# Performance work log

Hardware: AMD Instinct MI355X
Metric: run time of the kernel (lower is better)

The kernel has to match this reference:

```python
import jax, jax.numpy as jnp
import numpy as np
import math

EPSILON = 1e-15
N, D = 1048576, 128

def setup_inputs() -> dict:
    key = jax.random.key(0)
    k_x, k_mu, k_a, k_eps = jax.random.split(key, 4)
    X = jax.random.normal(k_x, (N, D), dtype=jnp.float32)
    # mu = (rand(D) - 0.5) * 2.0  as in __init__
    mu = (jax.random.uniform(k_mu, (D,), dtype=jnp.float32) - 0.5) * 2.0
    # sigma starts as identity; make a well-conditioned SPD matrix (as after EM updates)
    A = jax.random.normal(k_a, (D, D), dtype=jnp.float32) * 0.05
    sigma = jnp.eye(D, dtype=jnp.float32) + A @ A.T
    # epsilon property: (rand(D,D) - 0.5) * 1e-15, sampled once here (deterministic)
    eps = (jax.random.uniform(k_eps, (D, D), dtype=jnp.float32) - 0.5) * EPSILON
    return {"X": X, "mu": mu, "sigma": sigma, "eps": eps}

def reference(X, mu, sigma, eps):
    D_ = X.shape[1]
    log_two_pi_dims = D_ * (jnp.log(jnp.float32(2.0)) + jnp.log(jnp.float32(math.pi)))
    sig = sigma + eps
    inv_sigma = jnp.linalg.pinv(sig)
    _, log_det_sigma = jnp.linalg.slogdet(sig)
    log_den = 0.5 * (log_two_pi_dims + log_det_sigma)
    diff = X - mu  # [N, D]
    # batched quadratic form: diff @ inv_sigma . diff, summed over D
    quad = jnp.einsum('nd,de,ne->n', diff, inv_sigma, diff)  # [N]
    log_prob = -0.5 * quad - log_den  # [N]
    # nll=True path: return -log_prob, shape [N, 1] to match torch.cat of (1,1) blocks
    return (-log_prob)[:, None]
```

## Files before the change

kernel.cpp:

```cpp
#include <hip/hip_runtime.h>
#include <hip/hip_bf16.h>

typedef __bf16 bf16x8 __attribute__((ext_vector_type(8)));
typedef float f32x4 __attribute__((ext_vector_type(4)));

#define DIM 128
#define LOG_2PI 1.8378770664093453f
#define X0C 0.36f

__device__ __forceinline__ unsigned short f2bf(float f) {
    unsigned int u = __float_as_uint(f);
    u += 0x7FFFu + ((u >> 16) & 1u);
    return (unsigned short)(u >> 16);
}
__device__ __forceinline__ float bfu(unsigned short u) {
    return __uint_as_float((unsigned int)u << 16);
}
__device__ __forceinline__ int foidx(int r, int c) {
    return ((r >> 3) << 10) + (c << 3) + (r & 7);
}

__device__ __forceinline__ void mm_acc8(const unsigned short* __restrict__ Ps,
                                        const unsigned short* __restrict__ Qs,
                                        f32x4 acc[2][4], int wr, int tcb, int l15, int l4)
{
#pragma unroll
    for (int kk = 0; kk < 4; ++kk) {
        const int kc = kk * 4 + l4;
        const bf16x8 a0 = *reinterpret_cast<const bf16x8*>(Ps + (kc << 10) + ((wr * 32 + l15) << 3));
        const bf16x8 a1 = *reinterpret_cast<const bf16x8*>(Ps + (kc << 10) + ((wr * 32 + 16 + l15) << 3));
#pragma unroll
        for (int c = 0; c < 4; ++c) {
            const bf16x8 b = *reinterpret_cast<const bf16x8*>(Qs + (kc << 10) + (((tcb + c) * 16 + l15) << 3));
            acc[0][c] = __builtin_amdgcn_mfma_f32_16x16x32_bf16(a0, b, acc[0][c], 0, 0, 0);
            acc[1][c] = __builtin_amdgcn_mfma_f32_16x16x32_bf16(a1, b, acc[1][c], 0, 0, 0);
        }
    }
}

__device__ __forceinline__ void zacc(f32x4 acc[2][4]) {
#pragma unroll
    for (int rt = 0; rt < 2; ++rt)
#pragma unroll
        for (int c = 0; c < 4; ++c) { acc[rt][c][0] = 0.f; acc[rt][c][1] = 0.f; acc[rt][c][2] = 0.f; acc[rt][c][3] = 0.f; }
}

__device__ __forceinline__ void wb8s(unsigned short* __restrict__ C, f32x4 acc[2][4],
                                     int wr, int tcb, int l15, int l4, float sgn)
{
#pragma unroll
    for (int rt = 0; rt < 2; ++rt) {
        const int r0 = wr * 32 + rt * 16 + l4 * 4;
#pragma unroll
        for (int c = 0; c < 4; ++c) {
            ushort4 p;
            p.x = f2bf(sgn * acc[rt][c][0]); p.y = f2bf(sgn * acc[rt][c][1]);
            p.z = f2bf(sgn * acc[rt][c][2]); p.w = f2bf(sgn * acc[rt][c][3]);
            *reinterpret_cast<ushort4*>(&C[foidx(r0, (tcb + c) * 16 + l15)]) = p;
        }
    }
}

__global__ __launch_bounds__(512) void gm_setup(
    const float* __restrict__ sigma, const float* __restrict__ eps,
    unsigned short* __restrict__ wsB, float* __restrict__ wsScal)
{
    __shared__ __align__(16) unsigned short B0[16384];
    __shared__ __align__(16) unsigned short B1[16384];
    __shared__ __align__(16) unsigned short B2[16384];
    __shared__ __align__(16) unsigned short B3[16384];
    __shared__ float sv[8];

    const int tid  = threadIdx.x;
    const int lane = tid & 63;
    const int w    = tid >> 6;
    const int l15  = lane & 15;
    const int l4   = lane >> 4;
    const int wr   = w >> 1;
    const int tcb  = (w & 1) * 4;

#pragma unroll
    for (int h = 0; h < 4; ++h) {
        const int v = tid + h * 512;
        const int c = v & 127, rb = v >> 7;
        ushort4 s0, s1, x0q, x1q;
#pragma unroll
        for (int j = 0; j < 8; ++j) {
            const int r = rb * 8 + j;
            const float s = sigma[r * DIM + c] + eps[r * DIM + c];
            const float x = ((r == c) ? (2.0f * X0C) : 0.0f) - (X0C * X0C) * s;
            if (j < 4) { ((unsigned short*)&s0)[j] = f2bf(s); ((unsigned short*)&x0q)[j] = f2bf(x); }
            else       { ((unsigned short*)&s1)[j-4] = f2bf(s); ((unsigned short*)&x1q)[j-4] = f2bf(x); }
        }
        const int f = v * 8;
        *reinterpret_cast<ushort4*>(&B0[f])     = s0;
        *reinterpret_cast<ushort4*>(&B0[f + 4]) = s1;
        *reinterpret_cast<ushort4*>(&B2[f])     = x0q;
        *reinterpret_cast<ushort4*>(&B2[f + 4]) = x1q;
    }
    __syncthreads();

    for (int it = 0; it < 5; ++it) {
        unsigned short* Xc = (it & 1) ? B1 : B2;
        unsigned short* Xo = (it & 1) ? B2 : B1;
        f32x4 acc[2][4];
        zacc(acc);
        mm_acc8(B0, Xc, acc, wr, tcb, l15, l4);
        wb8s(B3, acc, wr, tcb, l15, l4, -1.0f);
        __syncthreads();
        f32x4 a2[2][4];
#pragma unroll
        for (int rt = 0; rt < 2; ++rt) {
            const int r0 = wr * 32 + rt * 16 + l4 * 4;
#pragma unroll
            for (int c = 0; c < 4; ++c) {
                const ushort4 x4 = *reinterpret_cast<const ushort4*>(&Xc[foidx(r0, (tcb + c) * 16 + l15)]);
                a2[rt][c][0] = 2.0f * bfu(x4.x); a2[rt][c][1] = 2.0f * bfu(x4.y);
                a2[rt][c][2] = 2.0f * bfu(x4.z); a2[rt][c][3] = 2.0f * bfu(x4.w);
            }
        }
        mm_acc8(Xc, B3, a2, wr, tcb, l15, l4);
        wb8s(Xo, a2, wr, tcb, l15, l4, 1.0f);
        __syncthreads();
    }

    float tsum = 0.0f;
#pragma unroll
    for (int h = 0; h < 4; ++h) {
        const int v = tid + h * 512;
        const int c = v & 127, rb = v >> 7;
        const int f = v * 8;
#pragma unroll
        for (int q = 0; q < 2; ++q) {
            const ushort4 wq = *reinterpret_cast<const ushort4*>(&B1[f + q * 4]);
            ushort4 mv;
#pragma unroll
            for (int j = 0; j < 4; ++j) {
                const int r = rb * 8 + q * 4 + j;
                const float wv = bfu(((const unsigned short*)&wq)[j]);
                const float mf = ((r == c) ? 1.0f : 0.0f) - wv;
                ((unsigned short*)&mv)[j] = f2bf(mf);
                tsum += 0.5f * mf * mf + ((r == c) ? mf : 0.0f);
            }
            *reinterpret_cast<ushort4*>(&B2[f + q * 4]) = mv;
            *reinterpret_cast<ushort4*>(&B3[f + q * 4]) = mv;
            *reinterpret_cast<ushort4*>(&wsB[f + q * 4]) = wq;
        }
    }
    __syncthreads();

    ushort4 pold[2][4];
    {
        f32x4 acc[2][4];
        zacc(acc);
        mm_acc8(B2, B3, acc, wr, tcb, l15, l4);
#pragma unroll
        for (int rt = 0; rt < 2; ++rt) {
            const int r0 = wr * 32 + rt * 16 + l4 * 4;
#pragma unroll
            for (int c = 0; c < 4; ++c) {
                const int f = foidx(r0, (tcb + c) * 16 + l15);
                const ushort4 m4 = *reinterpret_cast<const ushort4*>(&B2[f]);
                ushort4 nw;
#pragma unroll
                for (int j4 = 0; j4 < 4; ++j4) {
                    const float x = acc[rt][c][j4];
                    ((unsigned short*)&nw)[j4] = f2bf(x);
                    tsum += x * bfu(((const unsigned short*)&m4)[j4]) * 0.333333333f + x * x * 0.25f;
                }
                *reinterpret_cast<ushort4*>(&B0[f]) = nw;
                pold[rt][c] = nw;
            }
        }
        __syncthreads();
    }

    {
        f32x4 acc[2][4];
        zacc(acc);
        mm_acc8(B2, B0, acc, wr, tcb, l15, l4);
#pragma unroll
        for (int rt = 0; rt < 2; ++rt) {
            const int r0 = wr * 32 + rt * 16 + l4 * 4;
#pragma unroll
            for (int c = 0; c < 4; ++c) {
                const int f = foidx(r0, (tcb + c) * 16 + l15);
                ushort4 nw;
#pragma unroll
                for (int j4 = 0; j4 < 4; ++j4) {
                    const float x = acc[rt][c][j4];
                    ((unsigned short*)&nw)[j4] = f2bf(x);
                    tsum += x * bfu(((const unsigned short*)&pold[rt][c])[j4]) * 0.2f + x * x * 0.166666667f;
                }
                *reinterpret_cast<ushort4*>(&B3[f]) = nw;
                pold[rt][c] = nw;
            }
        }
        __syncthreads();
    }

    {
        f32x4 acc[2][4];
        zacc(acc);
        mm_acc8(B2, B3, acc, wr, tcb, l15, l4);
#pragma unroll
        for (int rt = 0; rt < 2; ++rt)
#pragma unroll
            for (int c = 0; c < 4; ++c)
#pragma unroll
                for (int j4 = 0; j4 < 4; ++j4) {
                    const float x = acc[rt][c][j4];
                    tsum += x * bfu(((const unsigned short*)&pold[rt][c])[j4]) * 0.142857143f + x * x * 0.125f;
                }
    }

    {
        float s = tsum;
#pragma unroll
        for (int off = 1; off < 64; off <<= 1) s += __shfl_xor(s, off, 64);
        if (lane == 0) sv[w] = s;
    }
    __syncthreads();
    if (tid == 0) {
        float tot = 0.f;
        for (int i = 0; i < 8; ++i) tot += sv[i];
        wsScal[0] = 0.5f * ((float)DIM * LOG_2PI + tot);
    }
}

__global__ __launch_bounds__(256) void gm_main(
    const float* __restrict__ X, const float* __restrict__ mu,
    const __hip_bfloat16* __restrict__ wsB, const float* __restrict__ wsScal,
    float* __restrict__ out, int ntiles)
{
    __shared__ __hip_bfloat16 sB[16 * 1024];
    __shared__ unsigned short sA[64 * 128];
    __shared__ float s_mu[DIM];

    const int tid  = threadIdx.x;
    const int lane = tid & 63;
    const int wave = tid >> 6;
    const int l15  = lane & 15;
    const int l4   = lane >> 4;

    {
        const float4* bg = reinterpret_cast<const float4*>(wsB);
        float4* bs = reinterpret_cast<float4*>(sB);
#pragma unroll
        for (int i = 0; i < 8; ++i) bs[tid + i * 256] = bg[tid + i * 256];
        if (tid < DIM) s_mu[tid] = mu[tid];
    }
    const float logden = wsScal[0];
    __syncthreads();

    for (int t = blockIdx.x; t < ntiles; t += gridDim.x) {
        const float4* xg = reinterpret_cast<const float4*>(X + (size_t)t * (64 * DIM));
#pragma unroll
        for (int i = 0; i < 8; ++i) {
            const int idx = tid + i * 256;
            const int r  = idx >> 5;
            const int c4 = idx & 31;
            float4 v = xg[idx];
            v.x -= s_mu[c4 * 4 + 0];
            v.y -= s_mu[c4 * 4 + 1];
            v.z -= s_mu[c4 * 4 + 2];
            v.w -= s_mu[c4 * 4 + 3];
            ushort4 b;
            b.x = f2bf(v.x); b.y = f2bf(v.y); b.z = f2bf(v.z); b.w = f2bf(v.w);
            char* p = (char*)sA + r * 256 + ((((c4 >> 1) ^ (r & 7)) << 4) | ((c4 & 1) << 3));
            *reinterpret_cast<ushort4*>(p) = b;
        }
        __syncthreads();

        f32x4 acc[8];
#pragma unroll
        for (int c = 0; c < 8; ++c) { acc[c][0] = 0.f; acc[c][1] = 0.f; acc[c][2] = 0.f; acc[c][3] = 0.f; }

        const int arow = wave * 16 + l15;
        const char* aBase = (const char*)sA + arow * 256;
#pragma unroll
        for (int kk = 0; kk < 4; ++kk) {
            const int kchunk = kk * 4 + l4;
            bf16x8 af = *reinterpret_cast<const bf16x8*>(aBase + ((kchunk ^ (arow & 7)) << 4));
            const __hip_bfloat16* bbase = sB + kchunk * 1024 + l15 * 8;
#pragma unroll
            for (int c = 0; c < 8; ++c) {
                bf16x8 bf = *reinterpret_cast<const bf16x8*>(bbase + c * 128);
                acc[c] = __builtin_amdgcn_mfma_f32_16x16x32_bf16(af, bf, acc[c], 0, 0, 0);
            }
        }

        float q0 = 0.f, q1 = 0.f, q2 = 0.f, q3 = 0.f;
#pragma unroll
        for (int c = 0; c < 8; ++c) {
            const int d = c * 16 + l15;
#pragma unroll
            for (int j = 0; j < 4; ++j) {
                const int r = wave * 16 + l4 * 4 + j;
                const int byt = r * 256 +
                    ((((d >> 3) ^ (r & 7)) << 4) | (((d >> 2) & 1) << 3) | ((d & 3) << 1));
                const unsigned short u = *reinterpret_cast<const unsigned short*>((const char*)sA + byt);
                const float df = __uint_as_float((unsigned int)u << 16);
                if (j == 0) q0 += acc[c][0] * df;
                else if (j == 1) q1 += acc[c][1] * df;
                else if (j == 2) q2 += acc[c][2] * df;
                else q3 += acc[c][3] * df;
            }
        }
#pragma unroll
        for (int off = 1; off < 16; off <<= 1) {
            q0 += __shfl_xor(q0, off, 64);
            q1 += __shfl_xor(q1, off, 64);
            q2 += __shfl_xor(q2, off, 64);
            q3 += __shfl_xor(q3, off, 64);
        }
        if (l15 == 0) {
            float4 o;
            o.x = 0.5f * q0 + logden;
            o.y = 0.5f * q1 + logden;
            o.z = 0.5f * q2 + logden;
            o.w = 0.5f * q3 + logden;
            *reinterpret_cast<float4*>(out + (size_t)t * 64 + wave * 16 + l4 * 4) = o;
        }
        __syncthreads();
    }
}

extern "C" void kernel_launch(void* const* d_in, const int* in_sizes, int n_in,
                              void* d_out, int out_size, void* d_ws, size_t ws_size,
                              hipStream_t stream) {
    const float* X     = (const float*)d_in[0];
    const float* mu    = (const float*)d_in[1];
    const float* sigma = (const float*)d_in[2];
    const float* eps   = (const float*)d_in[3];
    float* out = (float*)d_out;

    unsigned short* wsB = (unsigned short*)d_ws;
    float* wsScal = (float*)((char*)d_ws + 32768);

    const int N = in_sizes[0] / DIM;
    const int ntiles = N / 64;

    hipLaunchKernelGGL(gm_setup, dim3(1), dim3(512), 0, stream, sigma, eps, wsB, wsScal);

    const int grid = ntiles < 768 ? ntiles : 768;
    hipLaunchKernelGGL(gm_main, dim3(grid), dim3(256), 0, stream,
                       X, mu, (const __hip_bfloat16*)wsB, wsScal, out, ntiles);
}
```

Baseline: 124.6 us.

## Use inverse square root factor so quadratic form becomes sum of squares

The setup kernel now runs a coupled Newton-Schulz iteration that produces a scaled inverse square root of sigma instead of the inverse, and stores that as the GEMM operand. The main kernel then computes the quadratic form as the squared norm of the MFMA output, dropping the second pass that re-read diff from shared memory. Each wave now loads and uses its own 16-row slice of shared memory, which removes the block-wide barriers per tile. The risk is precision: the coupled iteration is done in bf16 with only four steps, and the log-determinant series is now fed a different matrix.

```diff
diff --git a/kernel.cpp b/kernel.cpp
--- a/kernel.cpp
+++ b/kernel.cpp
@@ -6,7 +6,8 @@
 
 #define DIM 128
 #define LOG_2PI 1.8378770664093453f
-#define X0C 0.36f
+#define INVLAM 0.3846153846f
+#define RSLAM  0.6201736729f
 
 __device__ __forceinline__ unsigned short f2bf(float f) {
     unsigned int u = __float_as_uint(f);
@@ -45,8 +46,8 @@
         for (int c = 0; c < 4; ++c) { acc[rt][c][0] = 0.f; acc[rt][c][1] = 0.f; acc[rt][c][2] = 0.f; acc[rt][c][3] = 0.f; }
 }
 
-__device__ __forceinline__ void wb8s(unsigned short* __restrict__ C, f32x4 acc[2][4],
-                                     int wr, int tcb, int l15, int l4, float sgn)
+__device__ __forceinline__ void wb8(unsigned short* __restrict__ C, f32x4 acc[2][4],
+                                    int wr, int tcb, int l15, int l4)
 {
 #pragma unroll
     for (int rt = 0; rt < 2; ++rt) {
@@ -54,8 +55,8 @@
 #pragma unroll
         for (int c = 0; c < 4; ++c) {
             ushort4 p;
-            p.x = f2bf(sgn * acc[rt][c][0]); p.y = f2bf(sgn * acc[rt][c][1]);
-            p.z = f2bf(sgn * acc[rt][c][2]); p.w = f2bf(sgn * acc[rt][c][3]);
+            p.x = f2bf(acc[rt][c][0]); p.y = f2bf(acc[rt][c][1]);
+            p.z = f2bf(acc[rt][c][2]); p.w = f2bf(acc[rt][c][3]);
             *reinterpret_cast<ushort4*>(&C[foidx(r0, (tcb + c) * 16 + l15)]) = p;
         }
     }
@@ -83,92 +84,118 @@
     for (int h = 0; h < 4; ++h) {
         const int v = tid + h * 512;
         const int c = v & 127, rb = v >> 7;
-        ushort4 s0, s1, x0q, x1q;
+        ushort4 a0q, a1q, z0q, z1q;
 #pragma unroll
         for (int j = 0; j < 8; ++j) {
             const int r = rb * 8 + j;
-            const float s = sigma[r * DIM + c] + eps[r * DIM + c];
-            const float x = ((r == c) ? (2.0f * X0C) : 0.0f) - (X0C * X0C) * s;
-            if (j < 4) { ((unsigned short*)&s0)[j] = f2bf(s); ((unsigned short*)&x0q)[j] = f2bf(x); }
-            else       { ((unsigned short*)&s1)[j-4] = f2bf(s); ((unsigned short*)&x1q)[j-4] = f2bf(x); }
+            const float a = (sigma[r * DIM + c] + eps[r * DIM + c]) * INVLAM;
+            const float z = 0.5f * (((r == c) ? 3.0f : 0.0f) - a);
+            if (j < 4) { ((unsigned short*)&a0q)[j] = f2bf(a); ((unsigned short*)&z0q)[j] = f2bf(z); }
+            else       { ((unsigned short*)&a1q)[j-4] = f2bf(a); ((unsigned short*)&z1q)[j-4] = f2bf(z); }
         }
         const int f = v * 8;
-        *reinterpret_cast<ushort4*>(&B0[f])     = s0;
-        *reinterpret_cast<ushort4*>(&B0[f + 4]) = s1;
-        *reinterpret_cast<ushort4*>(&B2[f])     = x0q;
-        *reinterpret_cast<ushort4*>(&B2[f + 4]) = x1q;
+        *reinterpret_cast<ushort4*>(&B0[f])     = a0q;
+        *reinterpret_cast<ushort4*>(&B0[f + 4]) = a1q;
+        *reinterpret_cast<ushort4*>(&B1[f])     = z0q;
+        *reinterpret_cast<ushort4*>(&B1[f + 4]) = z1q;
     }
     __syncthreads();
 
-    for (int it = 0; it < 5; ++it) {
-        unsigned short* Xc = (it & 1) ? B1 : B2;
-        unsigned short* Xo = (it & 1) ? B2 : B1;
-        f32x4 acc[2][4];
-        zacc(acc);
-        mm_acc8(B0, Xc, acc, wr, tcb, l15, l4);
-        wb8s(B3, acc, wr, tcb, l15, l4, -1.0f);
-        __syncthreads();
-        f32x4 a2[2][4];
+    for (int it = 0; it < 4; ++it) {
+        unsigned short* Zc = (it & 1) ? B2 : B1;
+        unsigned short* Zo = (it & 1) ? B1 : B2;
+        f32x4 acc[2][4];
+        zacc(acc);
+        mm_acc8(Zc, Zc, acc, wr, tcb, l15, l4);
+        wb8(Zo, acc, wr, tcb, l15, l4);
+        __syncthreads();
+        f32x4 av[2][4];
+        zacc(av);
+        mm_acc8(B0, Zo, av, wr, tcb, l15, l4);
+        {
+            f32x4 tp[2][4];
+#pragma unroll
+            for (int rt = 0; rt < 2; ++rt) {
+                const int r0 = wr * 32 + rt * 16 + l4 * 4;
+#pragma unroll
+                for (int c = 0; c < 4; ++c) {
+                    const int col = (tcb + c) * 16 + l15;
+#pragma unroll
+                    for (int j = 0; j < 4; ++j)
+                        tp[rt][c][j] = 0.5f * (((r0 + j == col) ? 3.0f : 0.0f) - av[rt][c][j]);
+                }
+            }
+            wb8(B3, tp, wr, tcb, l15, l4);
+        }
+        __syncthreads();
+        f32x4 az[2][4];
+        zacc(az);
+        mm_acc8(Zc, B3, az, wr, tcb, l15, l4);
+        wb8(Zo, az, wr, tcb, l15, l4);
+        __syncthreads();
+    }
+
+    for (int i = tid; i < 2048; i += 512) {
+        const ushort4 za = *reinterpret_cast<const ushort4*>(&B1[i * 8]);
+        const ushort4 zb = *reinterpret_cast<const ushort4*>(&B1[i * 8 + 4]);
+        ushort4 ba, bb;
+        ba.x = f2bf(bfu(za.x) * RSLAM); ba.y = f2bf(bfu(za.y) * RSLAM);
+        ba.z = f2bf(bfu(za.z) * RSLAM); ba.w = f2bf(bfu(za.w) * RSLAM);
+        bb.x = f2bf(bfu(zb.x) * RSLAM); bb.y = f2bf(bfu(zb.y) * RSLAM);
+        bb.z = f2bf(bfu(zb.z) * RSLAM); bb.w = f2bf(bfu(zb.w) * RSLAM);
+        *reinterpret_cast<ushort4*>(&B2[i * 8])     = ba;
+        *reinterpret_cast<ushort4*>(&B2[i * 8 + 4]) = bb;
+        *reinterpret_cast<ushort4*>(&wsB[i * 8])     = ba;
+        *reinterpret_cast<ushort4*>(&wsB[i * 8 + 4]) = bb;
+    }
+    __syncthreads();
+
+    float tsum = 0.0f;
+    ushort4 pold[2][4];
+    {
+        f32x4 acc[2][4];
+        zacc(acc);
+        mm_acc8(B2, B2, acc, wr, tcb, l15, l4);
 #pragma unroll
         for (int rt = 0; rt < 2; ++rt) {
             const int r0 = wr * 32 + rt * 16 + l4 * 4;
 #pragma unroll
             for (int c = 0; c < 4; ++c) {
-                const ushort4 x4 = *reinterpret_cast<const ushort4*>(&Xc[foidx(r0, (tcb + c) * 16 + l15)]);
-                a2[rt][c][0] = 2.0f * bfu(x4.x); a2[rt][c][1] = 2.0f * bfu(x4.y);
-                a2[rt][c][2] = 2.0f * bfu(x4.z); a2[rt][c][3] = 2.0f * bfu(x4.w);
-            }
-        }
-        mm_acc8(Xc, B3, a2, wr, tcb, l15, l4);
-        wb8s(Xo, a2, wr, tcb, l15, l4, 1.0f);
-        __syncthreads();
-    }
-
-    float tsum = 0.0f;
-#pragma unroll
-    for (int h = 0; h < 4; ++h) {
-        const int v = tid + h * 512;
-        const int c = v & 127, rb = v >> 7;
-        const int f = v * 8;
-#pragma unroll
-        for (int q = 0; q < 2; ++q) {
-            const ushort4 wq = *reinterpret_cast<const ushort4*>(&B1[f + q * 4]);
-            ushort4 mv;
-#pragma unroll
-            for (int j = 0; j < 4; ++j) {
-                const int r = rb * 8 + q * 4 + j;
-                const float wv = bfu(((const unsigned short*)&wq)[j]);
-                const float mf = ((r == c) ? 1.0f : 0.0f) - wv;
-                ((unsigned short*)&mv)[j] = f2bf(mf);
-                tsum += 0.5f * mf * mf + ((r == c) ? mf : 0.0f);
-            }
-            *reinterpret_cast<ushort4*>(&B2[f + q * 4]) = mv;
-            *reinterpret_cast<ushort4*>(&B3[f + q * 4]) = mv;
-            *reinterpret_cast<ushort4*>(&wsB[f + q * 4]) = wq;
-        }
-    }
-    __syncthreads();
-
-    ushort4 pold[2][4];
-    {
-        f32x4 acc[2][4];
-        zacc(acc);
-        mm_acc8(B2, B3, acc, wr, tcb, l15, l4);
+                const int col = (tcb + c) * 16 + l15;
+                const int f = foidx(r0, col);
+                ushort4 mv;
+#pragma unroll
+                for (int j = 0; j < 4; ++j) {
+                    const float mf = ((r0 + j == col) ? 1.0f : 0.0f) - acc[rt][c][j];
+                    ((unsigned short*)&mv)[j] = f2bf(mf);
+                    tsum += 0.5f * mf * mf + ((r0 + j == col) ? mf : 0.0f);
+                }
+                *reinterpret_cast<ushort4*>(&B0[f]) = mv;
+                *reinterpret_cast<ushort4*>(&B3[f]) = mv;
+                pold[rt][c] = mv;
+            }
+        }
+        __syncthreads();
+    }
+
+    {
+        f32x4 acc[2][4];
+        zacc(acc);
+        mm_acc8(B0, B3, acc, wr, tcb, l15, l4);
 #pragma unroll
         for (int rt = 0; rt < 2; ++rt) {
             const int r0 = wr * 32 + rt * 16 + l4 * 4;
 #pragma unroll
             for (int c = 0; c < 4; ++c) {
                 const int f = foidx(r0, (tcb + c) * 16 + l15);
-                const ushort4 m4 = *reinterpret_cast<const ushort4*>(&B2[f]);
                 ushort4 nw;
 #pragma unroll
                 for (int j4 = 0; j4 < 4; ++j4) {
                     const float x = acc[rt][c][j4];
                     ((unsigned short*)&nw)[j4] = f2bf(x);
-                    tsum += x * bfu(((const unsigned short*)&m4)[j4]) * 0.333333333f + x * x * 0.25f;
-                }
-                *reinterpret_cast<ushort4*>(&B0[f]) = nw;
+                    tsum += x * bfu(((const unsigned short*)&pold[rt][c])[j4]) * 0.333333333f + x * x * 0.25f;
+                }
+                *reinterpret_cast<ushort4*>(&B2[f]) = nw;
                 pold[rt][c] = nw;
             }
         }
@@ -178,7 +205,7 @@
     {
         f32x4 acc[2][4];
         zacc(acc);
-        mm_acc8(B2, B0, acc, wr, tcb, l15, l4);
+        mm_acc8(B0, B2, acc, wr, tcb, l15, l4);
 #pragma unroll
         for (int rt = 0; rt < 2; ++rt) {
             const int r0 = wr * 32 + rt * 16 + l4 * 4;
@@ -202,7 +229,7 @@
     {
         f32x4 acc[2][4];
         zacc(acc);
-        mm_acc8(B2, B3, acc, wr, tcb, l15, l4);
+        mm_acc8(B0, B3, acc, wr, tcb, l15, l4);
 #pragma unroll
         for (int rt = 0; rt < 2; ++rt)
 #pragma unroll
@@ -253,11 +280,14 @@
     const float logden = wsScal[0];
     __syncthreads();
 
+    char* const slice = (char*)sA + wave * 4096;
+    const char* const aBase = slice + l15 * 256;
+
     for (int t = blockIdx.x; t < ntiles; t += gridDim.x) {
-        const float4* xg = reinterpret_cast<const float4*>(X + (size_t)t * (64 * DIM));
+        const float4* xg = reinterpret_cast<const float4*>(X) + (size_t)t * 2048 + wave * 512;
 #pragma unroll
         for (int i = 0; i < 8; ++i) {
-            const int idx = tid + i * 256;
+            const int idx = lane + i * 64;
             const int r  = idx >> 5;
             const int c4 = idx & 31;
             float4 v = xg[idx];
@@ -267,25 +297,21 @@
             v.w -= s_mu[c4 * 4 + 3];
             ushort4 b;
             b.x = f2bf(v.x); b.y = f2bf(v.y); b.z = f2bf(v.z); b.w = f2bf(v.w);
-            char* p = (char*)sA + r * 256 + ((((c4 >> 1) ^ (r & 7)) << 4) | ((c4 & 1) << 3));
-            *reinterpret_cast<ushort4*>(p) = b;
-        }
-        __syncthreads();
+            *reinterpret_cast<ushort4*>(slice + r * 256 +
+                ((((c4 >> 1) ^ (r & 7)) << 4) | ((c4 & 1) << 3))) = b;
+        }
 
         f32x4 acc[8];
 #pragma unroll
         for (int c = 0; c < 8; ++c) { acc[c][0] = 0.f; acc[c][1] = 0.f; acc[c][2] = 0.f; acc[c][3] = 0.f; }
-
-        const int arow = wave * 16 + l15;
-        const char* aBase = (const char*)sA + arow * 256;
 #pragma unroll
         for (int kk = 0; kk < 4; ++kk) {
             const int kchunk = kk * 4 + l4;
-            bf16x8 af = *reinterpret_cast<const bf16x8*>(aBase + ((kchunk ^ (arow & 7)) << 4));
+            const bf16x8 af = *reinterpret_cast<const bf16x8*>(aBase + ((kchunk ^ (l15 & 7)) << 4));
             const __hip_bfloat16* bbase = sB + kchunk * 1024 + l15 * 8;
 #pragma unroll
             for (int c = 0; c < 8; ++c) {
-                bf16x8 bf = *reinterpret_cast<const bf16x8*>(bbase + c * 128);
+                const bf16x8 bf = *reinterpret_cast<const bf16x8*>(bbase + c * 128);
                 acc[c] = __builtin_amdgcn_mfma_f32_16x16x32_bf16(af, bf, acc[c], 0, 0, 0);
             }
         }
@@ -293,19 +319,10 @@
         float q0 = 0.f, q1 = 0.f, q2 = 0.f, q3 = 0.f;
 #pragma unroll
         for (int c = 0; c < 8; ++c) {
-            const int d = c * 16 + l15;
-#pragma unroll
-            for (int j = 0; j < 4; ++j) {
-                const int r = wave * 16 + l4 * 4 + j;
-                const int byt = r * 256 +
-                    ((((d >> 3) ^ (r & 7)) << 4) | (((d >> 2) & 1) << 3) | ((d & 3) << 1));
-                const unsigned short u = *reinterpret_cast<const unsigned short*>((const char*)sA + byt);
-                const float df = __uint_as_float((unsigned int)u << 16);
-                if (j == 0) q0 += acc[c][0] * df;
-                else if (j == 1) q1 += acc[c][1] * df;
-                else if (j == 2) q2 += acc[c][2] * df;
-                else q3 += acc[c][3] * df;
-            }
+            q0 += acc[c][0] * acc[c][0];
+            q1 += acc[c][1] * acc[c][1];
+            q2 += acc[c][2] * acc[c][2];
+            q3 += acc[c][3] * acc[c][3];
         }
 #pragma unroll
         for (int off = 1; off < 16; off <<= 1) {
@@ -322,7 +339,6 @@
             o.w = 0.5f * q3 + logden;
             *reinterpret_cast<float4*>(out + (size_t)t * 64 + wave * 16 + l4 * 4) = o;
         }
-        __syncthreads();
     }
 }
 
```

After: 131.8 us. 5.8% more time.
